# Kernel tuning notes

Measured on AMD Instinct MI355X. Metric: run time of the kernel, lower is better.

The kernel has to match this reference:

```python
import jax, jax.numpy as jnp
import numpy as np

BATCH = 2048
BUCKETS = 100000
DIM = 64

def setup_inputs() -> dict:
    key = jax.random.key(0)
    k1, k2 = jax.random.split(key)
    inputs = jax.random.uniform(k1, (BATCH, BUCKETS), dtype=jnp.float32)
    embeddings = jax.random.normal(k2, (BUCKETS, DIM), dtype=jnp.float32)
    return {"inputs": inputs, "embeddings": embeddings}

def reference(inputs, embeddings):
    # K.dot(inputs, embeddings): [B, buckets] @ [buckets, dim] -> [B, dim]
    out = jnp.matmul(inputs, embeddings)
    # mean=True branch: divide by count of active buckets, zero where empty
    s = jnp.sum(inputs, axis=-1, keepdims=True)  # [B, 1]
    out = jnp.where(s > 0, out / s, jnp.zeros_like(out))
    return out
```

## Files before the change

kernel.cpp:

```cpp
#include <hip/hip_runtime.h>
#include <hip/hip_bf16.h>

#define BATCH 2048
#define KDIM  100000
#define DIM   64
#define NKB   (KDIM / 32)
#define KP    32
#define ROWS_PER_BLOCK 64

typedef __attribute__((ext_vector_type(8))) short  short8;
typedef __attribute__((ext_vector_type(4))) float  f32x4;

__device__ __forceinline__ unsigned short f2bf(float f) {
    union { float f; unsigned int u; } v; v.f = f;
    unsigned int u = v.u;
    u += 0x7FFFu + ((u >> 16) & 1u);
    return (unsigned short)(u >> 16);
}

__global__ __launch_bounds__(256)
void hashemb_pack(const float* __restrict__ emb, unsigned short* __restrict__ pB) {
    const int kb   = blockIdx.x;
    const int t    = threadIdx.x >> 6;
    const int lane = threadIdx.x & 63;
    const int col  = t * 16 + (lane & 15);
    const int krow = kb * 32 + (lane >> 4) * 8;

    short8 w;
    #pragma unroll
    for (int j = 0; j < 8; ++j)
        w[j] = (short)f2bf(emb[(size_t)(krow + j) * DIM + col]);

    *(short8*)&pB[(((size_t)kb * 4 + t) * 64 + lane) * 8] = w;
}

__global__ __launch_bounds__(256, 4)
void hashemb_matmul(const float* __restrict__ inp,
                    const unsigned short* __restrict__ pB,
                    float* __restrict__ out_acc,
                    float* __restrict__ row_sum) {
    const int tid  = threadIdx.x;
    const int lane = tid & 63;
    const int wid  = tid >> 6;
    const int rb   = blockIdx.x;
    const int kp   = blockIdx.y;

    const int rowbase = rb * ROWS_PER_BLOCK + wid * 16;
    const int arow    = rowbase + (lane & 15);
    const int kgrp    = lane >> 4;

    const int base = NKB / KP;
    const int rem  = NKB % KP;
    const int cnt  = base + (kp < rem ? 1 : 0);
    const int kb0  = kp * base + (kp < rem ? kp : rem);

    const float* ap = inp + (size_t)arow * KDIM + (size_t)kb0 * 32 + kgrp * 8;
    const unsigned short* bp = pB + ((size_t)kb0 * 4 * 64 + lane) * 8;

    f32x4 acc[4];
    #pragma unroll
    for (int t = 0; t < 4; ++t) acc[t] = (f32x4)0.0f;
    float lsum = 0.0f;

    auto loadA = [&](int idx, f32x4& xa, f32x4& xb) {
        const int c = (idx < cnt) ? idx : cnt - 1;
        xa = *(const f32x4*)(ap + (size_t)c * 32);
        xb = *(const f32x4*)(ap + (size_t)c * 32 + 4);
    };

    auto consume = [&](int idx, f32x4& xa, f32x4& xb) {
        if (idx < cnt) {
            short8 af;
            #pragma unroll
            for (int j = 0; j < 4; ++j) {
                af[j]     = (short)f2bf(xa[j]);
                af[4 + j] = (short)f2bf(xb[j]);
            }
            lsum += xa[0] + xa[1] + xa[2] + xa[3]
                  + xb[0] + xb[1] + xb[2] + xb[3];
            const unsigned short* b = bp + (size_t)idx * 2048;
            #pragma unroll
            for (int t = 0; t < 4; ++t) {
                const short8 bf = *(const short8*)(b + t * 512);
                acc[t] = __builtin_amdgcn_mfma_f32_16x16x32_bf16(af, bf, acc[t], 0, 0, 0);
            }
        }
    };

    f32x4 a0a, a0b, a1a, a1b, a2a, a2b, a3a, a3b;
    f32x4 b0a, b0b, b1a, b1b, b2a, b2b, b3a, b3b;

    loadA(0, a0a, a0b); loadA(1, a1a, a1b);
    loadA(2, a2a, a2b); loadA(3, a3a, a3b);

    for (int g = 0; g < cnt; g += 8) {
        loadA(g + 4, b0a, b0b); loadA(g + 5, b1a, b1b);
        loadA(g + 6, b2a, b2b); loadA(g + 7, b3a, b3b);

        consume(g + 0, a0a, a0b); consume(g + 1, a1a, a1b);
        consume(g + 2, a2a, a2b); consume(g + 3, a3a, a3b);

        loadA(g + 8,  a0a, a0b); loadA(g + 9,  a1a, a1b);
        loadA(g + 10, a2a, a2b); loadA(g + 11, a3a, a3b);

        consume(g + 4, b0a, b0b); consume(g + 5, b1a, b1b);
        consume(g + 6, b2a, b2b); consume(g + 7, b3a, b3b);
    }

    lsum += __shfl_xor(lsum, 16, 64);
    lsum += __shfl_xor(lsum, 32, 64);
    if (lane < 16) atomicAdd(&row_sum[rowbase + lane], lsum);

    #pragma unroll
    for (int t = 0; t < 4; ++t) {
        const int col = t * 16 + (lane & 15);
        #pragma unroll
        for (int j = 0; j < 4; ++j) {
            const int row = rowbase + kgrp * 4 + j;
            atomicAdd(&out_acc[row * DIM + col], acc[t][j]);
        }
    }
}

__global__ __launch_bounds__(256)
void hashemb_finalize(float* __restrict__ out, const float* __restrict__ row_sum) {
    const int idx = blockIdx.x * blockDim.x + threadIdx.x;
    if (idx < BATCH * DIM) {
        const float s = row_sum[idx >> 6];
        const float o = out[idx];
        out[idx] = (s > 0.0f) ? (o / s) : 0.0f;
    }
}

extern "C" void kernel_launch(void* const* d_in, const int* in_sizes, int n_in,
                              void* d_out, int out_size, void* d_ws, size_t ws_size,
                              hipStream_t stream) {
    const float* inp = (const float*)d_in[0];
    const float* emb = (const float*)d_in[1];
    float* out = (float*)d_out;
    float* rs  = (float*)d_ws;
    unsigned short* pB = (unsigned short*)((char*)d_ws + 8192);

    hipMemsetAsync(out, 0, (size_t)BATCH * DIM * sizeof(float), stream);
    hipMemsetAsync(rs,  0, (size_t)BATCH * sizeof(float), stream);

    hashemb_pack<<<NKB, 256, 0, stream>>>(emb, pB);

    dim3 grid(BATCH / ROWS_PER_BLOCK, KP);
    hashemb_matmul<<<grid, 256, 0, stream>>>(inp, pB, out, rs);

    hashemb_finalize<<<(BATCH * DIM + 255) / 256, 256, 0, stream>>>(out, rs);
}
```

Before: 240.4 us.

## Replace atomic split-K with partial buffers, 32-row waves, XCD-aware block mapping

```diff
diff --git a/kernel.cpp b/kernel.cpp
--- a/kernel.cpp
+++ b/kernel.cpp
@@ -5,8 +5,9 @@
 #define KDIM  100000
 #define DIM   64
 #define NKB   (KDIM / 32)
-#define KP    32
-#define ROWS_PER_BLOCK 64
+#define KP    64
+#define RPB   128
+#define NRB   (BATCH / RPB)
 
 typedef __attribute__((ext_vector_type(8))) short  short8;
 typedef __attribute__((ext_vector_type(4))) float  f32x4;
@@ -37,99 +38,118 @@
 __global__ __launch_bounds__(256, 4)
 void hashemb_matmul(const float* __restrict__ inp,
                     const unsigned short* __restrict__ pB,
-                    float* __restrict__ out_acc,
-                    float* __restrict__ row_sum) {
+                    float* __restrict__ part,
+                    float* __restrict__ rsp) {
     const int tid  = threadIdx.x;
     const int lane = tid & 63;
     const int wid  = tid >> 6;
-    const int rb   = blockIdx.x;
-    const int kp   = blockIdx.y;
 
-    const int rowbase = rb * ROWS_PER_BLOCK + wid * 16;
-    const int arow    = rowbase + (lane & 15);
-    const int kgrp    = lane >> 4;
+    const int wg  = blockIdx.x;
+    const int xcd = wg & 7;
+    const int pos = wg >> 3;
+    const int kp  = xcd * (KP / 8) + (pos >> 4);
+    const int rb  = pos & 15;
 
     const int base = NKB / KP;
     const int rem  = NKB % KP;
     const int cnt  = base + (kp < rem ? 1 : 0);
     const int kb0  = kp * base + (kp < rem ? kp : rem);
 
-    const float* ap = inp + (size_t)arow * KDIM + (size_t)kb0 * 32 + kgrp * 8;
+    const int rowbase = rb * RPB + wid * 32;
+    const int r0   = rowbase + (lane & 15);
+    const int kgrp = lane >> 4;
+
+    const float* ap0 = inp + (size_t)r0 * KDIM + (size_t)kb0 * 32 + kgrp * 8;
+    const float* ap1 = ap0 + (size_t)16 * KDIM;
     const unsigned short* bp = pB + ((size_t)kb0 * 4 * 64 + lane) * 8;
 
-    f32x4 acc[4];
+    f32x4 acc0[4], acc1[4];
     #pragma unroll
-    for (int t = 0; t < 4; ++t) acc[t] = (f32x4)0.0f;
-    float lsum = 0.0f;
+    for (int t = 0; t < 4; ++t) { acc0[t] = (f32x4)0.0f; acc1[t] = (f32x4)0.0f; }
+    float lsum0 = 0.0f, lsum1 = 0.0f;
 
-    auto loadA = [&](int idx, f32x4& xa, f32x4& xb) {
-        const int c = (idx < cnt) ? idx : cnt - 1;
-        xa = *(const f32x4*)(ap + (size_t)c * 32);
-        xb = *(const f32x4*)(ap + (size_t)c * 32 + 4);
+    auto loadA = [&](int c, f32x4& xa, f32x4& xb, f32x4& ya, f32x4& yb) {
+        const int cc = (c < cnt) ? c : cnt - 1;
+        xa = *(const f32x4*)(ap0 + (size_t)cc * 32);
+        xb = *(const f32x4*)(ap0 + (size_t)cc * 32 + 4);
+        ya = *(const f32x4*)(ap1 + (size_t)cc * 32);
+        yb = *(const f32x4*)(ap1 + (size_t)cc * 32 + 4);
     };
 
-    auto consume = [&](int idx, f32x4& xa, f32x4& xb) {
-        if (idx < cnt) {
-            short8 af;
+    auto step = [&](int c, f32x4& xa, f32x4& xb, f32x4& ya, f32x4& yb) {
+        if (c < cnt) {
+            short8 af0, af1;
             #pragma unroll
             for (int j = 0; j < 4; ++j) {
-                af[j]     = (short)f2bf(xa[j]);
-                af[4 + j] = (short)f2bf(xb[j]);
+                af0[j] = (short)f2bf(xa[j]);  af0[4 + j] = (short)f2bf(xb[j]);
+                af1[j] = (short)f2bf(ya[j]);  af1[4 + j] = (short)f2bf(yb[j]);
             }
-            lsum += xa[0] + xa[1] + xa[2] + xa[3]
-                  + xb[0] + xb[1] + xb[2] + xb[3];
-            const unsigned short* b = bp + (size_t)idx * 2048;
+            lsum0 += xa[0] + xa[1] + xa[2] + xa[3] + xb[0] + xb[1] + xb[2] + xb[3];
+            lsum1 += ya[0] + ya[1] + ya[2] + ya[3] + yb[0] + yb[1] + yb[2] + yb[3];
+            loadA(c + 2, xa, xb, ya, yb);
+            const unsigned short* b = bp + (size_t)c * 2048;
             #pragma unroll
             for (int t = 0; t < 4; ++t) {
                 const short8 bf = *(const short8*)(b + t * 512);
-                acc[t] = __builtin_amdgcn_mfma_f32_16x16x32_bf16(af, bf, acc[t], 0, 0, 0);
+                acc0[t] = __builtin_amdgcn_mfma_f32_16x16x32_bf16(af0, bf, acc0[t], 0, 0, 0);
+                acc1[t] = __builtin_amdgcn_mfma_f32_16x16x32_bf16(af1, bf, acc1[t], 0, 0, 0);
             }
         }
     };
 
-    f32x4 a0a, a0b, a1a, a1b, a2a, a2b, a3a, a3b;
-    f32x4 b0a, b0b, b1a, b1b, b2a, b2b, b3a, b3b;
+    f32x4 x0a, x0b, y0a, y0b;
+    f32x4 x1a, x1b, y1a, y1b;
+    loadA(0, x0a, x0b, y0a, y0b);
+    loadA(1, x1a, x1b, y1a, y1b);
 
-    loadA(0, a0a, a0b); loadA(1, a1a, a1b);
-    loadA(2, a2a, a2b); loadA(3, a3a, a3b);
-
-    for (int g = 0; g < cnt; g += 8) {
-        loadA(g + 4, b0a, b0b); loadA(g + 5, b1a, b1b);
-        loadA(g + 6, b2a, b2b); loadA(g + 7, b3a, b3b);
-
-        consume(g + 0, a0a, a0b); consume(g + 1, a1a, a1b);
-        consume(g + 2, a2a, a2b); consume(g + 3, a3a, a3b);
-
-        loadA(g + 8,  a0a, a0b); loadA(g + 9,  a1a, a1b);
-        loadA(g + 10, a2a, a2b); loadA(g + 11, a3a, a3b);
-
-        consume(g + 4, b0a, b0b); consume(g + 5, b1a, b1b);
-        consume(g + 6, b2a, b2b); consume(g + 7, b3a, b3b);
+    for (int c = 0; c < cnt; c += 2) {
+        step(c,     x0a, x0b, y0a, y0b);
+        step(c + 1, x1a, x1b, y1a, y1b);
     }
 
-    lsum += __shfl_xor(lsum, 16, 64);
-    lsum += __shfl_xor(lsum, 32, 64);
-    if (lane < 16) atomicAdd(&row_sum[rowbase + lane], lsum);
+    lsum0 += __shfl_xor(lsum0, 16, 64);
+    lsum0 += __shfl_xor(lsum0, 32, 64);
+    lsum1 += __shfl_xor(lsum1, 16, 64);
+    lsum1 += __shfl_xor(lsum1, 32, 64);
+    if (lane < 16) {
+        rsp[(size_t)kp * BATCH + rowbase + lane]      = lsum0;
+        rsp[(size_t)kp * BATCH + rowbase + 16 + lane] = lsum1;
+    }
 
+    float* po = part + (size_t)kp * BATCH * DIM;
     #pragma unroll
     for (int t = 0; t < 4; ++t) {
         const int col = t * 16 + (lane & 15);
         #pragma unroll
         for (int j = 0; j < 4; ++j) {
             const int row = rowbase + kgrp * 4 + j;
-            atomicAdd(&out_acc[row * DIM + col], acc[t][j]);
+            po[(size_t)row * DIM + col]        = acc0[t][j];
+            po[(size_t)(row + 16) * DIM + col] = acc1[t][j];
         }
     }
 }
 
 __global__ __launch_bounds__(256)
-void hashemb_finalize(float* __restrict__ out, const float* __restrict__ row_sum) {
-    const int idx = blockIdx.x * blockDim.x + threadIdx.x;
-    if (idx < BATCH * DIM) {
-        const float s = row_sum[idx >> 6];
-        const float o = out[idx];
-        out[idx] = (s > 0.0f) ? (o / s) : 0.0f;
-    }
+void hashemb_rsreduce(const float* __restrict__ rsp, float* __restrict__ rs) {
+    const int row = blockIdx.x * 256 + threadIdx.x;
+    float s = 0.0f;
+    #pragma unroll 8
+    for (int p = 0; p < KP; ++p) s += rsp[(size_t)p * BATCH + row];
+    rs[row] = s;
+}
+
+__global__ __launch_bounds__(256)
+void hashemb_finalize(const float* __restrict__ part, const float* __restrict__ rs,
+                      float* __restrict__ out) {
+    const int i4 = blockIdx.x * 256 + threadIdx.x;
+    const float s = rs[i4 >> 4];
+    f32x4 o = (f32x4)0.0f;
+    #pragma unroll 8
+    for (int p = 0; p < KP; ++p)
+        o += *(const f32x4*)(part + (size_t)p * BATCH * DIM + (size_t)i4 * 4);
+    const float inv = (s > 0.0f) ? (1.0f / s) : 0.0f;
+    o *= inv;
+    *(f32x4*)(out + (size_t)i4 * 4) = o;
 }
 
 extern "C" void kernel_launch(void* const* d_in, const int* in_sizes, int n_in,
@@ -138,16 +158,17 @@
     const float* inp = (const float*)d_in[0];
     const float* emb = (const float*)d_in[1];
     float* out = (float*)d_out;
+
     float* rs  = (float*)d_ws;
-    unsigned short* pB = (unsigned short*)((char*)d_ws + 8192);
-
-    hipMemsetAsync(out, 0, (size_t)BATCH * DIM * sizeof(float), stream);
-    hipMemsetAsync(rs,  0, (size_t)BATCH * sizeof(float), stream);
+    float* rsp = (float*)((char*)d_ws + 8192);
+    float* part = (float*)((char*)d_ws + 532480);
+    unsigned short* pB = (unsigned short*)((char*)d_ws + 34086912);
 
     hashemb_pack<<<NKB, 256, 0, stream>>>(emb, pB);
 
-    dim3 grid(BATCH / ROWS_PER_BLOCK, KP);
-    hashemb_matmul<<<grid, 256, 0, stream>>>(inp, pB, out, rs);
+    hashemb_matmul<<<NRB * KP, 256, 0, stream>>>(inp, pB, part, rsp);
 
-    hashemb_finalize<<<(BATCH * DIM + 255) / 256, 256, 0, stream>>>(out, rs);
+    hashemb_rsreduce<<<BATCH / 256, 256, 0, stream>>>(rsp, rs);
+
+    hashemb_finalize<<<(BATCH * DIM / 4) / 256, 256, 0, stream>>>(part, rs, out);
 }
```

New measurement: 216.9 us. 1.11x faster.
